# Optimization experiments

Measured on AMD Instinct MI355X. Metric: run time of the kernel, lower is better.

Reference implementation:

```python
import jax, jax.numpy as jnp
import numpy as np

D_MODEL = 1024
NUM_HEADS = 16
D_K = D_MODEL // NUM_HEADS
D_FF = 4096
EPS = 1e-5


def _layernorm(x, gamma, beta):
    mu = jnp.mean(x, axis=-1, keepdims=True)
    var = jnp.mean(jnp.square(x - mu), axis=-1, keepdims=True)
    return (x - mu) * jax.lax.rsqrt(var + EPS) * gamma + beta


def setup_inputs() -> dict:
    key = jax.random.key(0)
    ks = jax.random.split(key, 16)
    B, S = 4, 2048
    s_in = 1.0 / np.sqrt(D_MODEL)
    s_ff = 1.0 / np.sqrt(D_FF)
    inp = {
        "x": jax.random.normal(ks[0], (B, S, D_MODEL), jnp.float32),
        "src_mask": jnp.ones((B, 1, 1, S), jnp.int32),
        "w_q": jax.random.normal(ks[1], (D_MODEL, D_MODEL), jnp.float32) * s_in,
        "b_q": jnp.zeros((D_MODEL,), jnp.float32),
        "w_k": jax.random.normal(ks[2], (D_MODEL, D_MODEL), jnp.float32) * s_in,
        "b_k": jnp.zeros((D_MODEL,), jnp.float32),
        "w_v": jax.random.normal(ks[3], (D_MODEL, D_MODEL), jnp.float32) * s_in,
        "b_v": jnp.zeros((D_MODEL,), jnp.float32),
        "w_o": jax.random.normal(ks[4], (D_MODEL, D_MODEL), jnp.float32) * s_in,
        "b_o": jnp.zeros((D_MODEL,), jnp.float32),
        "w1": jax.random.normal(ks[5], (D_MODEL, D_FF), jnp.float32) * s_in,
        "b1": jnp.zeros((D_FF,), jnp.float32),
        "w2": jax.random.normal(ks[6], (D_FF, D_MODEL), jnp.float32) * s_ff,
        "b2": jnp.zeros((D_MODEL,), jnp.float32),
        "g1": jnp.ones((D_MODEL,), jnp.float32),
        "be1": jnp.zeros((D_MODEL,), jnp.float32),
        "g2": jnp.ones((D_MODEL,), jnp.float32),
        "be2": jnp.zeros((D_MODEL,), jnp.float32),
    }
    return inp


def reference(x, src_mask, w_q, b_q, w_k, b_k, w_v, b_v, w_o, b_o,
              w1, b1, w2, b2, g1, be1, g2, be2):
    B, S, _ = x.shape

    def split_heads(t):  # [B,S,D] -> [B,H,S,dk]
        return t.reshape(B, S, NUM_HEADS, D_K).transpose(0, 2, 1, 3)

    q = split_heads(x @ w_q + b_q)
    k = split_heads(x @ w_k + b_k)
    v = split_heads(x @ w_v + b_v)

    scores = jnp.einsum("bhqd,bhkd->bhqk", q, k) / np.sqrt(D_K)
    scores = jnp.where(src_mask == 0, -jnp.inf, scores)
    attn = jax.nn.softmax(scores, axis=-1)
    ctx = jnp.einsum("bhqk,bhkd->bhqd", attn, v)
    merged = ctx.transpose(0, 2, 1, 3).reshape(B, S, D_MODEL)
    attn_out = merged @ w_o + b_o

    h = _layernorm(x + attn_out, g1, be1)
    ff = jax.nn.relu(h @ w1 + b1) @ w2 + b2
    return _layernorm(h + ff, g2, be2)
```

## Files before the change

### kernel.cpp

```cpp
#include <hip/hip_runtime.h>

typedef unsigned short u16;
typedef __attribute__((ext_vector_type(4))) unsigned short u16x4;
typedef __attribute__((ext_vector_type(8))) short bf16x8;
typedef __attribute__((ext_vector_type(4))) float f32x4;
typedef __attribute__((ext_vector_type(16))) float f32x16;

__device__ inline float bf2f(u16 u) {
  union { unsigned int i; float f; } v; v.i = ((unsigned int)u) << 16; return v.f;
}
__device__ inline u16 f2bf(float f) {
  union { float f; unsigned int i; } v; v.f = f;
  unsigned int r = v.i + 0x7fffu + ((v.i >> 16) & 1u);
  return (u16)(r >> 16);
}
__device__ inline unsigned int cvt_pk_bf16(float lo, float hi) {
  unsigned int r;
  asm("v_cvt_pk_bf16_f32 %0, %1, %2" : "=v"(r) : "v"(lo), "v"(hi));
  return r;
}
__device__ inline f32x16 zero16() {
  f32x16 z;
  #pragma unroll
  for (int i = 0; i < 16; ++i) z[i] = 0.f;
  return z;
}

typedef const __attribute__((address_space(1))) unsigned int* gas_t;
typedef __attribute__((address_space(3))) unsigned int* las_t;
__device__ inline void gload_lds16(const u16* g, u16* l) {
  __builtin_amdgcn_global_load_lds((gas_t)(unsigned long long)(const void*)g,
                                   (las_t)(unsigned int)(unsigned long long)(void*)l,
                                   16, 0, 0);
}

__global__ __launch_bounds__(256) void cvt_bf16(const float* __restrict__ src,
                                                u16* __restrict__ dst, int n) {
  int i = (blockIdx.x * 256 + threadIdx.x) * 4;
  if (i >= n) return;
  float4 v = *(const float4*)(src + i);
  u16x4 o;
  o.x = f2bf(v.x); o.y = f2bf(v.y); o.z = f2bf(v.z); o.w = f2bf(v.w);
  *(u16x4*)(dst + i) = o;
}

__global__ __launch_bounds__(256) void concat3(const float* __restrict__ a,
                                               const float* __restrict__ b,
                                               const float* __restrict__ c,
                                               float* __restrict__ o, int n) {
  int i = blockIdx.x * 256 + threadIdx.x;
  if (i >= n) return;
  o[i] = a[i]; o[n + i] = b[i]; o[2 * n + i] = c[i];
}

__global__ __launch_bounds__(256) void transpose_f32_bf16(const float* __restrict__ src,
                                                          u16* __restrict__ dst,
                                                          int R, int C) {
  __shared__ u16 tile[32][33];
  int tx = threadIdx.x & 31, ty = threadIdx.x >> 5;
  int c0 = blockIdx.x * 32, r0 = blockIdx.y * 32;
  #pragma unroll
  for (int i = ty; i < 32; i += 8)
    tile[i][tx] = f2bf(src[(size_t)(r0 + i) * C + c0 + tx]);
  __syncthreads();
  #pragma unroll
  for (int i = ty; i < 32; i += 8)
    dst[(size_t)(c0 + i) * R + r0 + tx] = tile[tx][i];
}

__global__ __launch_bounds__(256) void transpose_v(const u16* __restrict__ src,
                                                   u16* __restrict__ VT,
                                                   int B, int S, int H, int RS, int CO) {
  __shared__ u16 tile[32][33];
  int tx = threadIdx.x & 31, ty = threadIdx.x >> 5;
  int s0 = blockIdx.x * 32, d0 = blockIdx.y * 32;
  int bh = blockIdx.z;
  int b = bh / H, h = bh % H;
  #pragma unroll
  for (int i = ty; i < 32; i += 8)
    tile[i][tx] = src[(size_t)(b * S + s0 + i) * RS + CO + h * 64 + d0 + tx];
  __syncthreads();
  #pragma unroll
  for (int i = ty; i < 32; i += 8)
    VT[((size_t)bh * 64 + d0 + i) * S + s0 + tx] = tile[tx][i];
}

__global__ __launch_bounds__(256) void gemm_bt(const u16* __restrict__ A,
                                               const u16* __restrict__ Bt,
                                               const float* __restrict__ bias,
                                               u16* __restrict__ C,
                                               int M, int N, int K, int relu) {
  __shared__ u16 As[128 * 64];
  __shared__ u16 Bs[128 * 64];
  const int tid = threadIdx.x;
  const int lane = tid & 63, wid = tid >> 6;
  const int lr = lane & 15, quad = lane >> 4;
  const int wm = (wid >> 1) * 64, wn = (wid & 1) * 64;
  const int m0 = blockIdx.y * 128, n0 = blockIdx.x * 128;
  const int grow = lane >> 3;
  const int gcol = ((lane & 7) ^ grow) * 8;
  const int rsw = (lr & 7) << 3;

  f32x4 acc[4][4];
  const f32x4 zero = {0.f, 0.f, 0.f, 0.f};
  #pragma unroll
  for (int mt = 0; mt < 4; ++mt)
    #pragma unroll
    for (int nt = 0; nt < 4; ++nt) acc[mt][nt] = zero;

  for (int k0 = 0; k0 < K; k0 += 64) {
    #pragma unroll
    for (int it = 0; it < 4; ++it) {
      int rbase = wid * 32 + it * 8;
      gload_lds16(A + (size_t)(m0 + rbase + grow) * K + k0 + gcol, &As[rbase * 64]);
      gload_lds16(Bt + (size_t)(n0 + rbase + grow) * K + k0 + gcol, &Bs[rbase * 64]);
    }
    __syncthreads();
    #pragma unroll
    for (int kk = 0; kk < 2; ++kk) {
      bf16x8 af[4], bfr[4];
      #pragma unroll
      for (int mt = 0; mt < 4; ++mt)
        af[mt] = *(const bf16x8*)(&As[(wm + mt * 16 + lr) * 64 + ((kk * 32 + quad * 8) ^ rsw)]);
      #pragma unroll
      for (int nt = 0; nt < 4; ++nt)
        bfr[nt] = *(const bf16x8*)(&Bs[(wn + nt * 16 + lr) * 64 + ((kk * 32 + quad * 8) ^ rsw)]);
      #pragma unroll
      for (int mt = 0; mt < 4; ++mt)
        #pragma unroll
        for (int nt = 0; nt < 4; ++nt)
          acc[mt][nt] = __builtin_amdgcn_mfma_f32_16x16x32_bf16(af[mt], bfr[nt], acc[mt][nt], 0, 0, 0);
    }
    __syncthreads();
  }

  #pragma unroll
  for (int nt = 0; nt < 4; ++nt) {
    int n = n0 + wn + nt * 16 + lr;
    float bv = bias[n];
    #pragma unroll
    for (int mt = 0; mt < 4; ++mt) {
      #pragma unroll
      for (int i = 0; i < 4; ++i) {
        int m = m0 + wm + mt * 16 + quad * 4 + i;
        float v = acc[mt][nt][i] + bv;
        if (relu) v = fmaxf(v, 0.f);
        C[(size_t)m * N + n] = f2bf(v);
      }
    }
  }
}

__global__ __launch_bounds__(512, 2) void gemm256(const u16* __restrict__ A,
                                                  const u16* __restrict__ Bt,
                                                  const float* __restrict__ bias,
                                                  u16* __restrict__ C,
                                                  int M, int N, int K, int relu) {
  __shared__ u16 As[2][256][64];
  __shared__ u16 Bs[2][256][64];
  const int tid = threadIdx.x;
  const int lane = tid & 63, wid = tid >> 6;
  const int lr = lane & 15, quad = lane >> 4;
  const int wm2 = wid >> 2, wn4 = wid & 3;
  const int m0 = blockIdx.y * 256, n0 = blockIdx.x * 256;
  const int srl = lane >> 3;
  const int scol = ((lane & 7) ^ srl) * 8;
  const int rsw = (lr & 7) << 3;
  const int NT = K >> 6;

  f32x4 acc[8][4];
  #pragma unroll
  for (int mi = 0; mi < 8; ++mi)
    #pragma unroll
    for (int ni = 0; ni < 4; ++ni) {
      acc[mi][ni][0] = 0.f; acc[mi][ni][1] = 0.f;
      acc[mi][ni][2] = 0.f; acc[mi][ni][3] = 0.f;
    }

#define STAGE_A(TT, MQ)                                                        \
  if ((TT) < NT) {                                                             \
    int c2 = (TT) & 1, k0s = (TT) << 6;                                        \
    const u16* ga = A + (size_t)(m0 + (MQ) * 64 + wid * 8 + srl) * K + k0s + scol; \
    gload_lds16(ga, &As[c2][(MQ) * 64 + wid * 8][0]);                          \
    gload_lds16(ga + (size_t)128 * K, &As[c2][128 + (MQ) * 64 + wid * 8][0]);  \
  }
#define STAGE_B(TT, HH)                                                        \
  if ((TT) < NT) {                                                             \
    int c2 = (TT) & 1, k0s = (TT) << 6;                                        \
    const u16* gb = Bt + (size_t)(n0 + (HH) * 128 + wid * 8 + srl) * K + k0s + scol; \
    gload_lds16(gb, &Bs[c2][(HH) * 128 + wid * 8][0]);                         \
    gload_lds16(gb + (size_t)64 * K, &Bs[c2][(HH) * 128 + 64 + wid * 8][0]);   \
  }

#define PHASE(MQ, NQ, STAGE_STMT)                                              \
  {                                                                            \
    bf16x8 af[4][2], bfr[2][2];                                                \
    _Pragma("unroll")                                                          \
    for (int mt = 0; mt < 4; ++mt)                                             \
      _Pragma("unroll")                                                        \
      for (int kk = 0; kk < 2; ++kk)                                           \
        af[mt][kk] = *(const bf16x8*)(&As[c][wm2 * 128 + (MQ) * 64 + mt * 16 + lr] \
                                         [(kk * 32 + quad * 8) ^ rsw]);        \
    _Pragma("unroll")                                                          \
    for (int nt = 0; nt < 2; ++nt)                                             \
      _Pragma("unroll")                                                        \
      for (int kk = 0; kk < 2; ++kk)                                           \
        bfr[nt][kk] = *(const bf16x8*)(&Bs[c][wn4 * 64 + (NQ) * 32 + nt * 16 + lr] \
                                          [(kk * 32 + quad * 8) ^ rsw]);       \
    STAGE_STMT;                                                                \
    __builtin_amdgcn_s_barrier();                                              \
    __builtin_amdgcn_s_setprio(1);                                             \
    _Pragma("unroll")                                                          \
    for (int mt = 0; mt < 4; ++mt)                                             \
      _Pragma("unroll")                                                        \
      for (int nt = 0; nt < 2; ++nt)                                           \
        _Pragma("unroll")                                                      \
        for (int kk = 0; kk < 2; ++kk)                                         \
          acc[(MQ) * 4 + mt][(NQ) * 2 + nt] = __builtin_amdgcn_mfma_f32_16x16x32_bf16( \
              af[mt][kk], bfr[nt][kk], acc[(MQ) * 4 + mt][(NQ) * 2 + nt], 0, 0, 0); \
    __builtin_amdgcn_s_setprio(0);                                             \
    __builtin_amdgcn_s_barrier();                                              \
  }

  STAGE_A(0, 0);
  STAGE_A(0, 1);
  STAGE_B(0, 0);
  STAGE_B(0, 1);
  STAGE_A(1, 0);

  for (int t = 0; t < NT; ++t) {
    const int c = t & 1;
    if (t + 1 < NT) {
      asm volatile("s_waitcnt vmcnt(2)" ::: "memory");
    } else {
      asm volatile("s_waitcnt vmcnt(0)" ::: "memory");
    }
    __builtin_amdgcn_s_barrier();
    PHASE(0, 0, STAGE_A(t + 1, 1));
    PHASE(0, 1, STAGE_B(t + 1, 0));
    PHASE(1, 0, STAGE_B(t + 1, 1));
    PHASE(1, 1, STAGE_A(t + 2, 0));
  }
#undef PHASE
#undef STAGE_A
#undef STAGE_B

  #pragma unroll
  for (int ni = 0; ni < 4; ++ni) {
    int n = n0 + wn4 * 64 + ni * 16 + lr;
    float bv = bias[n];
    #pragma unroll
    for (int mi = 0; mi < 8; ++mi) {
      #pragma unroll
      for (int i = 0; i < 4; ++i) {
        int m = m0 + wm2 * 128 + mi * 16 + quad * 4 + i;
        float v = acc[mi][ni][i] + bv;
        if (relu) v = fmaxf(v, 0.f);
        C[(size_t)m * N + n] = f2bf(v);
      }
    }
  }
}

__global__ __launch_bounds__(256) void flash_attn(const u16* __restrict__ Qp,
                                                  const u16* __restrict__ Kp,
                                                  const u16* __restrict__ VT,
                                                  const int* __restrict__ mask,
                                                  u16* __restrict__ ctx,
                                                  int B, int S, int H, int QSTR) {
  __shared__ u16 kt_lds[64 * 64];
  __shared__ u16 vt_lds[64 * 64];
  const int tid = threadIdx.x;
  const int lane = tid & 63, wid = tid >> 6;
  const int l31 = lane & 31, hi = lane >> 5;
  const int bh = blockIdx.y;
  const int b = bh / H, h = bh % H;
  const u16* vt_base = VT + (size_t)bh * 64 * S;
  const int* mbase = mask + b * S;
  const float SC = 0.125f * 1.44269504089f;

  const int srl = lane >> 3;
  const int scol = ((lane & 7) ^ srl) * 8;
  const int rsw = (lane & 7) << 3;

  const int q = blockIdx.x * 128 + wid * 32 + l31;
  bf16x8 qf[4];
  {
    const u16* qptr = Qp + (size_t)(b * S + q) * QSTR + h * 64;
    #pragma unroll
    for (int t = 0; t < 4; ++t)
      qf[t] = *(const bf16x8*)(qptr + t * 16 + hi * 8);
  }

  float m_i = -1e30f, l_i = 0.f;
  f32x16 o0 = zero16(), o1 = zero16();

  const u16* kgp = Kp + ((size_t)b * S + wid * 16 + srl) * QSTR + h * 64 + scol;
  const u16* vgp = vt_base + (size_t)(wid * 16 + srl) * S + scol;
  u16* klb = &kt_lds[(wid * 16) * 64];
  u16* vlb = &vt_lds[(wid * 16) * 64];

  for (int kt = 0; kt < S; kt += 64) {
    gload_lds16(kgp + (size_t)kt * QSTR, klb);
    gload_lds16(kgp + (size_t)(kt + 8) * QSTR, klb + 8 * 64);
    gload_lds16(vgp + kt, vlb);
    gload_lds16(vgp + 8 * (size_t)S + kt, vlb + 8 * 64);
    int mv = mbase[kt + lane];
    unsigned long long bal = __ballot(mv != 0);
    __syncthreads();

    f32x16 sa0 = zero16(), sa1 = zero16();
    const u16* krow0 = &kt_lds[l31 * 64];
    const u16* krow1 = &kt_lds[(32 + l31) * 64];
    __builtin_amdgcn_s_setprio(1);
    #pragma unroll
    for (int dblock = 0; dblock < 4; ++dblock) {
      int c = (dblock * 16 + hi * 8) ^ rsw;
      bf16x8 kf0 = *(const bf16x8*)(krow0 + c);
      bf16x8 kf1 = *(const bf16x8*)(krow1 + c);
      sa0 = __builtin_amdgcn_mfma_f32_32x32x16_bf16(kf0, qf[dblock], sa0, 0, 0, 0);
      sa1 = __builtin_amdgcn_mfma_f32_32x32x16_bf16(kf1, qf[dblock], sa1, 0, 0, 0);
    }
    __builtin_amdgcn_s_setprio(0);

    if (bal != 0xFFFFFFFFFFFFFFFFull) {
      unsigned long long balh = bal >> (hi * 4);
      #pragma unroll
      for (int r = 0; r < 16; ++r) {
        int kloc = (r & 3) + 8 * (r >> 2);
        if (!((balh >> kloc) & 1)) sa0[r] = -2e30f;
        if (!((balh >> (32 + kloc)) & 1)) sa1[r] = -2e30f;
      }
    }

    float tmax = sa0[0];
    #pragma unroll
    for (int r = 1; r < 16; ++r) tmax = fmaxf(tmax, sa0[r]);
    #pragma unroll
    for (int r = 0; r < 16; ++r) tmax = fmaxf(tmax, sa1[r]);
    tmax = fmaxf(tmax, __shfl_xor(tmax, 32, 64));
    if (__any(tmax > m_i + 44.0f)) {
      float mn = fmaxf(m_i, tmax);
      float al = exp2f((m_i - mn) * SC);
      m_i = mn;
      l_i *= al;
      #pragma unroll
      for (int r = 0; r < 16; ++r) { o0[r] *= al; o1[r] *= al; }
    }
    float msc = m_i * SC;
    float rs = 0.f;
    #pragma unroll
    for (int r = 0; r < 16; ++r) {
      float p0 = exp2f(__builtin_fmaf(sa0[r], SC, -msc));
      float p1 = exp2f(__builtin_fmaf(sa1[r], SC, -msc));
      sa0[r] = p0; sa1[r] = p1; rs += p0 + p1;
    }
    l_i += rs;

    unsigned pfw[4][4];
    #pragma unroll
    for (int b1 = 0; b1 < 2; ++b1) {
      #pragma unroll
      for (int pair = 0; pair < 2; ++pair) {
        unsigned X0 = cvt_pk_bf16(sa0[(2 * b1) * 4 + pair * 2], sa0[(2 * b1) * 4 + pair * 2 + 1]);
        unsigned Y0 = cvt_pk_bf16(sa0[(2 * b1 + 1) * 4 + pair * 2], sa0[(2 * b1 + 1) * 4 + pair * 2 + 1]);
        unsigned Xp0 = __shfl_xor(X0, 32, 64);
        unsigned Yp0 = __shfl_xor(Y0, 32, 64);
        pfw[b1][pair] = hi ? Yp0 : X0;
        pfw[b1][pair + 2] = hi ? Y0 : Xp0;
        unsigned X1 = cvt_pk_bf16(sa1[(2 * b1) * 4 + pair * 2], sa1[(2 * b1) * 4 + pair * 2 + 1]);
        unsigned Y1 = cvt_pk_bf16(sa1[(2 * b1 + 1) * 4 + pair * 2], sa1[(2 * b1 + 1) * 4 + pair * 2 + 1]);
        unsigned Xp1 = __shfl_xor(X1, 32, 64);
        unsigned Yp1 = __shfl_xor(Y1, 32, 64);
        pfw[2 + b1][pair] = hi ? Yp1 : X1;
        pfw[2 + b1][pair + 2] = hi ? Y1 : Xp1;
      }
    }

    const u16* vrow0 = &vt_lds[l31 * 64];
    const u16* vrow1 = &vt_lds[(32 + l31) * 64];
    __builtin_amdgcn_s_setprio(1);
    #pragma unroll
    for (int kb = 0; kb < 4; ++kb) {
      int c = (kb * 16 + hi * 8) ^ rsw;
      bf16x8 vf0 = *(const bf16x8*)(vrow0 + c);
      bf16x8 vf1 = *(const bf16x8*)(vrow1 + c);
      union { unsigned w[4]; bf16x8 v; } pu;
      pu.w[0] = pfw[kb][0]; pu.w[1] = pfw[kb][1];
      pu.w[2] = pfw[kb][2]; pu.w[3] = pfw[kb][3];
      o0 = __builtin_amdgcn_mfma_f32_32x32x16_bf16(vf0, pu.v, o0, 0, 0, 0);
      o1 = __builtin_amdgcn_mfma_f32_32x32x16_bf16(vf1, pu.v, o1, 0, 0, 0);
    }
    __builtin_amdgcn_s_setprio(0);
    __syncthreads();
  }

  l_i += __shfl_xor(l_i, 32, 64);
  float linv = 1.f / fmaxf(l_i, 1e-30f);
  u16* op = ctx + (size_t)(b * S + q) * (H * 64) + h * 64;
  #pragma unroll
  for (int rq = 0; rq < 4; ++rq) {
    uint2 w0, w1;
    w0.x = cvt_pk_bf16(o0[rq * 4 + 0] * linv, o0[rq * 4 + 1] * linv);
    w0.y = cvt_pk_bf16(o0[rq * 4 + 2] * linv, o0[rq * 4 + 3] * linv);
    *(uint2*)(op + rq * 8 + hi * 4) = w0;
    w1.x = cvt_pk_bf16(o1[rq * 4 + 0] * linv, o1[rq * 4 + 1] * linv);
    w1.y = cvt_pk_bf16(o1[rq * 4 + 2] * linv, o1[rq * 4 + 3] * linv);
    *(uint2*)(op + 32 + rq * 8 + hi * 4) = w1;
  }
}

__device__ inline float block_reduce_sum(float v, float* sbuf) {
  #pragma unroll
  for (int m = 1; m < 64; m <<= 1) v += __shfl_xor(v, m, 64);
  int w = threadIdx.x >> 6;
  if ((threadIdx.x & 63) == 0) sbuf[w] = v;
  __syncthreads();
  v = sbuf[0] + sbuf[1] + sbuf[2] + sbuf[3];
  __syncthreads();
  return v;
}

__global__ __launch_bounds__(256) void add_ln(const float* __restrict__ a32,
                                              const u16* __restrict__ a16,
                                              const u16* __restrict__ b,
                                              const float* __restrict__ g,
                                              const float* __restrict__ be,
                                              u16* __restrict__ out16,
                                              float* __restrict__ out32, int D) {
  __shared__ float sbuf[4];
  int row = blockIdx.x;
  size_t base = (size_t)row * D;
  int i = threadIdx.x * 4;
  float v[4];
  {
    u16x4 bv = *(const u16x4*)(b + base + i);
    if (a32) {
      float4 av = *(const float4*)(a32 + base + i);
      v[0] = av.x + bf2f(bv.x); v[1] = av.y + bf2f(bv.y);
      v[2] = av.z + bf2f(bv.z); v[3] = av.w + bf2f(bv.w);
    } else {
      u16x4 av = *(const u16x4*)(a16 + base + i);
      v[0] = bf2f(av.x) + bf2f(bv.x); v[1] = bf2f(av.y) + bf2f(bv.y);
      v[2] = bf2f(av.z) + bf2f(bv.z); v[3] = bf2f(av.w) + bf2f(bv.w);
    }
  }
  float sum = v[0] + v[1] + v[2] + v[3];
  sum = block_reduce_sum(sum, sbuf);
  float mean = sum / (float)D;
  float var = 0.f;
  #pragma unroll
  for (int j = 0; j < 4; ++j) { float d = v[j] - mean; var += d * d; }
  var = block_reduce_sum(var, sbuf);
  float rstd = rsqrtf(var / (float)D + 1e-5f);
  float4 gv = *(const float4*)(g + i);
  float4 bev = *(const float4*)(be + i);
  float o0 = (v[0] - mean) * rstd * gv.x + bev.x;
  float o1 = (v[1] - mean) * rstd * gv.y + bev.y;
  float o2 = (v[2] - mean) * rstd * gv.z + bev.z;
  float o3 = (v[3] - mean) * rstd * gv.w + bev.w;
  if (out32) {
    float4 o = {o0, o1, o2, o3};
    *(float4*)(out32 + base + i) = o;
  } else {
    u16x4 o;
    o.x = f2bf(o0); o.y = f2bf(o1); o.z = f2bf(o2); o.w = f2bf(o3);
    *(u16x4*)(out16 + base + i) = o;
  }
}

extern "C" void kernel_launch(void* const* d_in, const int* in_sizes, int n_in,
                              void* d_out, int out_size, void* d_ws, size_t ws_size,
                              hipStream_t stream) {
  (void)in_sizes; (void)n_in; (void)out_size; (void)ws_size;
  const float* x   = (const float*)d_in[0];
  const int* mask  = (const int*)d_in[1];
  const float* wq  = (const float*)d_in[2];
  const float* bq  = (const float*)d_in[3];
  const float* wk  = (const float*)d_in[4];
  const float* bk  = (const float*)d_in[5];
  const float* wv  = (const float*)d_in[6];
  const float* bv  = (const float*)d_in[7];
  const float* wo  = (const float*)d_in[8];
  const float* bo  = (const float*)d_in[9];
  const float* w1  = (const float*)d_in[10];
  const float* b1  = (const float*)d_in[11];
  const float* w2  = (const float*)d_in[12];
  const float* b2  = (const float*)d_in[13];
  const float* g1  = (const float*)d_in[14];
  const float* be1 = (const float*)d_in[15];
  const float* g2  = (const float*)d_in[16];
  const float* be2 = (const float*)d_in[17];

  const int B = 4, S = 2048, D = 1024, H = 16, DFF = 4096;
  const int D3 = 3 * D;
  const size_t TOK = (size_t)B * S;
  const size_t TD = TOK * D;

  u16* ws   = (u16*)d_ws;
  u16* QKVp = ws;
  u16* xb   = ws + 3 * TD;
  u16* VT   = xb;
  u16* CTX  = ws + 4 * TD;
  u16* ATT  = ws + 5 * TD;
  u16* Hb   = ws + 6 * TD;
  u16* QKVT = ws + 7 * TD;
  u16* WOT  = QKVT + 3 * (size_t)D * D;
  u16* W1T  = WOT + (size_t)D * D;
  u16* FF1  = ws;
  u16* FF2  = ATT;
  u16* W2T  = QKVT;
  float* biasc = (float*)CTX;

  dim3 blk(256);

  cvt_bf16<<<dim3((unsigned)(TD / (256 * 4))), blk, 0, stream>>>(x, xb, (int)TD);
  concat3<<<dim3(4), blk, 0, stream>>>(bq, bk, bv, biasc, D);

  transpose_f32_bf16<<<dim3(D / 32, D / 32), blk, 0, stream>>>(wq, QKVT, D, D);
  transpose_f32_bf16<<<dim3(D / 32, D / 32), blk, 0, stream>>>(wk, QKVT + (size_t)D * D, D, D);
  transpose_f32_bf16<<<dim3(D / 32, D / 32), blk, 0, stream>>>(wv, QKVT + 2 * (size_t)D * D, D, D);
  transpose_f32_bf16<<<dim3(D / 32, D / 32), blk, 0, stream>>>(wo, WOT, D, D);
  transpose_f32_bf16<<<dim3(DFF / 32, D / 32), blk, 0, stream>>>(w1, W1T, D, DFF);

  gemm256<<<dim3(D3 / 256, TOK / 256), dim3(512), 0, stream>>>(
      xb, QKVT, biasc, QKVp, (int)TOK, D3, D, 0);

  transpose_v<<<dim3(S / 32, 2, B * H), blk, 0, stream>>>(QKVp, VT, B, S, H, D3, 2 * D);

  flash_attn<<<dim3(S / 128, B * H), blk, 0, stream>>>(
      QKVp, QKVp + D, VT, mask, CTX, B, S, H, D3);

  gemm_bt<<<dim3(D / 128, TOK / 128), blk, 0, stream>>>(CTX, WOT, bo, ATT, (int)TOK, D, D, 0);

  transpose_f32_bf16<<<dim3(D / 32, DFF / 32), blk, 0, stream>>>(w2, W2T, DFF, D);

  add_ln<<<dim3((unsigned)TOK), blk, 0, stream>>>(x, (const u16*)nullptr, ATT, g1, be1,
                                                  Hb, (float*)nullptr, D);

  gemm256<<<dim3(DFF / 256, TOK / 256), dim3(512), 0, stream>>>(
      Hb, W1T, b1, FF1, (int)TOK, DFF, D, 1);
  gemm_bt<<<dim3(D / 128, TOK / 128), blk, 0, stream>>>(FF1, W2T, b2, FF2, (int)TOK, D, DFF, 0);

  add_ln<<<dim3((unsigned)TOK), blk, 0, stream>>>((const float*)nullptr, Hb, FF2, g2, be2,
                                                  (u16*)nullptr, (float*)d_out, D);
}
```

Before: 626.6 us.

## Restructure GEMM main loop into unrolled two-tile pipeline with finer vmcnt waits

The GEMM main loop is unrolled by two K-tiles, and A fragments are reused across two N-subphases, so each A fragment set is loaded from LDS once per pair instead of once per phase. Global-to-LDS stage issue order is reshuffled, and partial s_waitcnt vmcnt waits are placed at the end of subphases, with a peeled epilogue for the last two tiles. The aim is to keep more loads in flight and cut LDS read traffic and barrier stalls. The cost is more complex hand-tuned wait counts, and the loop assumes NT is even and at least 2.

```diff
diff --git a/kernel.cpp b/kernel.cpp
--- a/kernel.cpp
+++ b/kernel.cpp
@@ -177,35 +177,35 @@
       acc[mi][ni][2] = 0.f; acc[mi][ni][3] = 0.f;
     }
 
-#define STAGE_A(TT, MQ)                                                        \
-  if ((TT) < NT) {                                                             \
-    int c2 = (TT) & 1, k0s = (TT) << 6;                                        \
-    const u16* ga = A + (size_t)(m0 + (MQ) * 64 + wid * 8 + srl) * K + k0s + scol; \
-    gload_lds16(ga, &As[c2][(MQ) * 64 + wid * 8][0]);                          \
-    gload_lds16(ga + (size_t)128 * K, &As[c2][128 + (MQ) * 64 + wid * 8][0]);  \
-  }
-#define STAGE_B(TT, HH)                                                        \
-  if ((TT) < NT) {                                                             \
-    int c2 = (TT) & 1, k0s = (TT) << 6;                                        \
-    const u16* gb = Bt + (size_t)(n0 + (HH) * 128 + wid * 8 + srl) * K + k0s + scol; \
-    gload_lds16(gb, &Bs[c2][(HH) * 128 + wid * 8][0]);                         \
-    gload_lds16(gb + (size_t)64 * K, &Bs[c2][(HH) * 128 + 64 + wid * 8][0]);   \
-  }
-
-#define PHASE(MQ, NQ, STAGE_STMT)                                              \
+  auto stageA = [&](int TT, int MQ) {
+    int c2 = TT & 1;
+    int k0s = TT << 6;
+    const u16* ga = A + (size_t)(m0 + MQ * 64 + wid * 8 + srl) * K + k0s + scol;
+    gload_lds16(ga, &As[c2][MQ * 64 + wid * 8][0]);
+    gload_lds16(ga + (size_t)128 * K, &As[c2][128 + MQ * 64 + wid * 8][0]);
+  };
+  auto stageB = [&](int TT, int HH) {
+    int c2 = TT & 1;
+    int k0s = TT << 6;
+    const u16* gb = Bt + (size_t)(n0 + HH * 128 + wid * 8 + srl) * K + k0s + scol;
+    gload_lds16(gb, &Bs[c2][HH * 128 + wid * 8][0]);
+    gload_lds16(gb + (size_t)64 * K, &Bs[c2][HH * 128 + 64 + wid * 8][0]);
+  };
+
+#define W4 asm volatile("s_waitcnt vmcnt(4)" ::: "memory")
+#define W6 asm volatile("s_waitcnt vmcnt(6)" ::: "memory")
+#define W2 asm volatile("s_waitcnt vmcnt(2)" ::: "memory")
+#define W0 asm volatile("s_waitcnt vmcnt(0)" ::: "memory")
+#define WN ((void)0)
+
+#define SUBPHASE(CC, MQ, NQ, STAGE_STMT, WAIT_STMT)                            \
   {                                                                            \
-    bf16x8 af[4][2], bfr[2][2];                                                \
-    _Pragma("unroll")                                                          \
-    for (int mt = 0; mt < 4; ++mt)                                             \
-      _Pragma("unroll")                                                        \
-      for (int kk = 0; kk < 2; ++kk)                                           \
-        af[mt][kk] = *(const bf16x8*)(&As[c][wm2 * 128 + (MQ) * 64 + mt * 16 + lr] \
-                                         [(kk * 32 + quad * 8) ^ rsw]);        \
+    bf16x8 bfr[2][2];                                                          \
     _Pragma("unroll")                                                          \
     for (int nt = 0; nt < 2; ++nt)                                             \
       _Pragma("unroll")                                                        \
       for (int kk = 0; kk < 2; ++kk)                                           \
-        bfr[nt][kk] = *(const bf16x8*)(&Bs[c][wn4 * 64 + (NQ) * 32 + nt * 16 + lr] \
+        bfr[nt][kk] = *(const bf16x8*)(&Bs[CC][wn4 * 64 + (NQ) * 32 + nt * 16 + lr] \
                                           [(kk * 32 + quad * 8) ^ rsw]);       \
     STAGE_STMT;                                                                \
     __builtin_amdgcn_s_barrier();                                              \
@@ -219,31 +219,51 @@
           acc[(MQ) * 4 + mt][(NQ) * 2 + nt] = __builtin_amdgcn_mfma_f32_16x16x32_bf16( \
               af[mt][kk], bfr[nt][kk], acc[(MQ) * 4 + mt][(NQ) * 2 + nt], 0, 0, 0); \
     __builtin_amdgcn_s_setprio(0);                                             \
+    WAIT_STMT;                                                                 \
     __builtin_amdgcn_s_barrier();                                              \
   }
 
-  STAGE_A(0, 0);
-  STAGE_A(0, 1);
-  STAGE_B(0, 0);
-  STAGE_B(0, 1);
-  STAGE_A(1, 0);
-
-  for (int t = 0; t < NT; ++t) {
-    const int c = t & 1;
-    if (t + 1 < NT) {
-      asm volatile("s_waitcnt vmcnt(2)" ::: "memory");
-    } else {
-      asm volatile("s_waitcnt vmcnt(0)" ::: "memory");
-    }
-    __builtin_amdgcn_s_barrier();
-    PHASE(0, 0, STAGE_A(t + 1, 1));
-    PHASE(0, 1, STAGE_B(t + 1, 0));
-    PHASE(1, 0, STAGE_B(t + 1, 1));
-    PHASE(1, 1, STAGE_A(t + 2, 0));
-  }
-#undef PHASE
-#undef STAGE_A
-#undef STAGE_B
+#define PAIR(CC, MQ, ST1, WT1, ST2, WT2)                                       \
+  {                                                                            \
+    bf16x8 af[4][2];                                                           \
+    _Pragma("unroll")                                                          \
+    for (int mt = 0; mt < 4; ++mt)                                             \
+      _Pragma("unroll")                                                        \
+      for (int kk = 0; kk < 2; ++kk)                                           \
+        af[mt][kk] = *(const bf16x8*)(&As[CC][wm2 * 128 + (MQ) * 64 + mt * 16 + lr] \
+                                         [(kk * 32 + quad * 8) ^ rsw]);        \
+    SUBPHASE(CC, MQ, 0, ST1, WT1)                                              \
+    SUBPHASE(CC, MQ, 1, ST2, WT2)                                              \
+  }
+
+  stageA(0, 0);
+  stageB(0, 0);
+  stageB(0, 1);
+  stageA(1, 0);
+  stageA(0, 1);
+  W4;
+  __builtin_amdgcn_s_barrier();
+
+  for (int t = 0; t + 2 < NT; t += 2) {
+    PAIR(0, 0, stageB(t + 1, 0), WN, stageB(t + 1, 1), W4)
+    PAIR(0, 1, stageA(t + 1, 1), WN, stageA(t + 2, 0), W4)
+    PAIR(1, 0, stageB(t + 2, 0), WN, stageB(t + 2, 1), W6)
+    PAIR(1, 1, stageA(t + 3, 0), WN, stageA(t + 2, 1), W4)
+  }
+  {
+    const int t = NT - 2;
+    PAIR(0, 0, stageB(t + 1, 0), WN, stageB(t + 1, 1), W4)
+    PAIR(0, 1, stageA(t + 1, 1), WN, WN, W2)
+    PAIR(1, 0, WN, WN, WN, W0)
+    PAIR(1, 1, WN, WN, WN, WN)
+  }
+#undef PAIR
+#undef SUBPHASE
+#undef W4
+#undef W6
+#undef W2
+#undef W0
+#undef WN
 
   #pragma unroll
   for (int ni = 0; ni < 4; ++ni) {
```

Result: faster. 609.2 us (-2.8%).
